# Performance work log

Measured on AMD Instinct MI355X. Metric: run time of the kernel, lower is better.

## Reference

```python
import jax, jax.numpy as jnp
import numpy as np

NUM_BANDS = 8
WINDOW = 2048
OVERLAP = 1024
SR = 16000


def _band_mask(L):
    # Replicates torch: band = searchsorted(band_ranges, |freq|, left) - 1.
    # DC bin gives band=-1 which torch negative-indexes into the LAST band,
    # hence the mod. All bins satisfy band < NUM_BANDS, so all are assigned.
    freqs = np.fft.fftfreq(L, 1.0 / SR)
    ranges = np.linspace(0.0, SR / 2.0, NUM_BANDS + 1)
    idx = np.searchsorted(ranges, np.abs(freqs), side='left') - 1
    idx = idx % NUM_BANDS
    mask = (idx[None, :] == np.arange(NUM_BANDS)[:, None]).astype(np.float32)
    return jnp.asarray(mask)  # [bands, L]


def _band_signals(x):
    # mag*exp(i*phase) of masked bins == masked complex bins; ifft().real per band
    L = x.shape[-1]
    X = jnp.fft.fft(x)                         # [B, L] complex
    mask = _band_mask(L)                       # [bands, L]
    Xb = X[:, None, :] * mask[None, :, :]      # [B, bands, L]
    return jnp.fft.ifft(Xb).real               # [B, bands, L]


def _chunks(sig):
    L = sig.shape[-1]
    hop = WINDOW - OVERLAP
    n = (L - OVERLAP) // hop                   # num_chunks (static)
    idx = (jnp.arange(n) * hop)[:, None] + jnp.arange(WINDOW)[None, :]  # [n, W]
    return sig[:, :, idx]                       # [B, bands, n, W]


def _loudness(x):
    # BS.1770-style energy loudness (vectorized stand-in for the repo's
    # undefined `loudness` helper): -0.691 + 10*log10(mean square)
    ms = jnp.mean(x * x, axis=-1)
    return -0.691 + 10.0 * jnp.log10(ms + 1e-12)


def reference(watermarked_signals, original_signals):
    ro = _band_signals(original_signals)
    rw = _band_signals(watermarked_signals)
    lo = _loudness(_chunks(ro))                # [B, bands, n]
    lw = _loudness(_chunks(rw))
    lo = jnp.where(jnp.isnan(lo), 0.0, lo)
    lw = jnp.where(jnp.isnan(lw), 0.0, lw)
    diff = (lw - lo).reshape(-1)               # ordered (i, j, k) like the torch loop
    w = jax.nn.softmax(diff)
    return jnp.sum(w * diff)


def setup_inputs() -> dict:
    key = jax.random.key(0)
    k1, k2 = jax.random.split(key)
    B, L = 8, 160000
    return {
        'watermarked_signals': jax.random.normal(k1, (B, L), dtype=jnp.float32),
        'original_signals': jax.random.normal(k2, (B, L), dtype=jnp.float32),
    }
```

## Files before the change

### kernel.cpp

```cpp
#include <hip/hip_runtime.h>
#include <hip/hip_fp16.h>
#include <math.h>

constexpr int L      = 160000;
constexpr int BATCH  = 8;
constexpr int NB     = 8;
constexpr int NHOPS  = 156;
constexpr int NCHUNK = 155;
constexpr int RS     = 289;
constexpr float TWO_PI = 6.28318530717958647692f;
constexpr float INVL = 1.0f / (float)L;

__device__ __forceinline__ float2 cmulf(float2 a, float2 b) {
  return make_float2(a.x * b.x - a.y * b.y, a.x * b.y + a.y * b.x);
}

__device__ __forceinline__ float2 cisf(float a) {
  float s, c;
  __sincosf(a, &s, &c);
  return make_float2(c, s);
}

__device__ __forceinline__ float2 conjf(float2 a) { return make_float2(a.x, -a.y); }

__device__ __forceinline__ int pad8(int i) { return i + (i >> 3); }

template <int SIGN>
__device__ __forceinline__ void bf4s(float2* v) {
  float2 t0 = make_float2(v[0].x + v[2].x, v[0].y + v[2].y);
  float2 t1 = make_float2(v[0].x - v[2].x, v[0].y - v[2].y);
  float2 t2 = make_float2(v[1].x + v[3].x, v[1].y + v[3].y);
  float2 t3 = make_float2(v[1].x - v[3].x, v[1].y - v[3].y);
  v[0] = make_float2(t0.x + t2.x, t0.y + t2.y);
  v[2] = make_float2(t0.x - t2.x, t0.y - t2.y);
  if constexpr (SIGN < 0) {
    v[1] = make_float2(t1.x + t3.y, t1.y - t3.x);
    v[3] = make_float2(t1.x - t3.y, t1.y + t3.x);
  } else {
    v[1] = make_float2(t1.x - t3.y, t1.y + t3.x);
    v[3] = make_float2(t1.x + t3.y, t1.y - t3.x);
  }
}

template <int SIGN>
__device__ __forceinline__ void bf5s(float2* v) {
  const float c1 = 0.30901699437494745f, s1 = 0.9510565162951535f;
  const float c2 = -0.8090169943749475f, s2 = 0.5877852522924731f;
  float2 t1 = make_float2(v[1].x + v[4].x, v[1].y + v[4].y);
  float2 t3 = make_float2(v[1].x - v[4].x, v[1].y - v[4].y);
  float2 t2 = make_float2(v[2].x + v[3].x, v[2].y + v[3].y);
  float2 t4 = make_float2(v[2].x - v[3].x, v[2].y - v[3].y);
  float2 a = make_float2(v[0].x + c1 * t1.x + c2 * t2.x, v[0].y + c1 * t1.y + c2 * t2.y);
  float2 b = make_float2(s1 * t3.x + s2 * t4.x, s1 * t3.y + s2 * t4.y);
  float2 c = make_float2(v[0].x + c2 * t1.x + c1 * t2.x, v[0].y + c2 * t1.y + c1 * t2.y);
  float2 d = make_float2(s2 * t3.x - s1 * t4.x, s2 * t3.y - s1 * t4.y);
  v[0] = make_float2(v[0].x + t1.x + t2.x, v[0].y + t1.y + t2.y);
  if constexpr (SIGN < 0) {
    v[1] = make_float2(a.x + b.y, a.y - b.x);
    v[4] = make_float2(a.x - b.y, a.y + b.x);
    v[2] = make_float2(c.x + d.y, c.y - d.x);
    v[3] = make_float2(c.x - d.y, c.y + d.x);
  } else {
    v[1] = make_float2(a.x - b.y, a.y + b.x);
    v[4] = make_float2(a.x + b.y, a.y - b.x);
    v[2] = make_float2(c.x - d.y, c.y + d.x);
    v[3] = make_float2(c.x + d.y, c.y - d.x);
  }
}

template <int R>
__device__ __forceinline__ void twchain(float2* v, float2 t1) {
  float2 t = t1;
  v[1] = cmulf(v[1], t);
#pragma unroll
  for (int r = 2; r < R; ++r) { t = cmulf(t, t1); v[r] = cmulf(v[r], t); }
}

__device__ __forceinline__ int rev3_5(int q) {
  int q5 = q / 5, q25 = q / 25;
  int d0 = q - 5 * q5, d1 = q5 - 5 * q25;
  return 25 * d0 + 5 * d1 + q25;
}

__device__ __forceinline__ int rev3_4(int q) {
  return ((q & 3) << 4) | (q & 12) | (q >> 4);
}

template <int SUB, int SIGN>
__device__ __forceinline__ void dif5_ip_stage_c(float2* a, int ln) {
  int i1 = ln, i2 = ln + 64;
  bool g2 = (i2 < 125);
  int j1 = i1 % SUB, j2 = i2 % SUB;
  int b1 = (i1 / SUB) * (5 * SUB) + j1;
  int b2 = (i2 / SUB) * (5 * SUB) + j2;
  float2 u[5], v[5];
#pragma unroll
  for (int r = 0; r < 5; ++r) u[r] = a[b1 + SUB * r];
  if (g2) {
#pragma unroll
    for (int r = 0; r < 5; ++r) v[r] = a[b2 + SUB * r];
  }
  bf5s<SIGN>(u);
  twchain<5>(u, cisf((float)SIGN * (TWO_PI / (float)(5 * SUB)) * (float)j1));
  if (g2) {
    bf5s<SIGN>(v);
    twchain<5>(v, cisf((float)SIGN * (TWO_PI / (float)(5 * SUB)) * (float)j2));
  }
#pragma unroll
  for (int r = 0; r < 5; ++r) a[b1 + SUB * r] = u[r];
  if (g2) {
#pragma unroll
    for (int r = 0; r < 5; ++r) a[b2 + SUB * r] = v[r];
  }
}

template <int SUB>
__device__ __forceinline__ void dif5_ip_stage_t(float2* a, int ln, float2 t1a, float2 t1b) {
  int i1 = ln, i2 = ln + 64;
  bool g2 = (i2 < 125);
  int j1 = i1 % SUB, j2 = i2 % SUB;
  int b1 = (i1 / SUB) * (5 * SUB) + j1;
  int b2 = (i2 / SUB) * (5 * SUB) + j2;
  float2 u[5], v[5];
#pragma unroll
  for (int r = 0; r < 5; ++r) u[r] = a[b1 + SUB * r];
  if (g2) {
#pragma unroll
    for (int r = 0; r < 5; ++r) v[r] = a[b2 + SUB * r];
  }
  bf5s<1>(u);
  twchain<5>(u, t1a);
  if (g2) {
    bf5s<1>(v);
    twchain<5>(v, t1b);
  }
#pragma unroll
  for (int r = 0; r < 5; ++r) a[b1 + SUB * r] = u[r];
  if (g2) {
#pragma unroll
    for (int r = 0; r < 5; ++r) a[b2 + SUB * r] = v[r];
  }
}

template <int SIGN>
__device__ __forceinline__ void dif625_ip(float2* a, int ln) {
  dif5_ip_stage_c<125, SIGN>(a, ln);
  dif5_ip_stage_c<25, SIGN>(a, ln);
  dif5_ip_stage_c<5, SIGN>(a, ln);
  int q1 = ln, q2 = ln + 64;
  bool g2 = (q2 < 125);
  float2 u[5], v[5];
#pragma unroll
  for (int r = 0; r < 5; ++r) u[r] = a[5 * q1 + r];
  if (g2) {
#pragma unroll
    for (int r = 0; r < 5; ++r) v[r] = a[5 * q2 + r];
  }
  bf5s<SIGN>(u);
  if (g2) bf5s<SIGN>(v);
  int rv1 = rev3_5(q1), rv2 = rev3_5(q2);
#pragma unroll
  for (int r = 0; r < 5; ++r) a[125 * r + rv1] = u[r];
  if (g2) {
#pragma unroll
    for (int r = 0; r < 5; ++r) a[125 * r + rv2] = v[r];
  }
}

template <int SIGN>
__device__ __forceinline__ void dif256sw_tw(float2* a, int ln,
                                            float2 tw1, float2 tw2, float2 tw3) {
  {
    int b = pad8(ln);
    float2 u[4];
#pragma unroll
    for (int r = 0; r < 4; ++r) u[r] = a[b + 72 * r];
    bf4s<SIGN>(u);
    twchain<4>(u, tw1);
#pragma unroll
    for (int r = 0; r < 4; ++r) a[b + 72 * r] = u[r];
  }
  {
    int j = ln & 15, b = pad8(64 * (ln >> 4) + j);
    float2 u[4];
#pragma unroll
    for (int r = 0; r < 4; ++r) u[r] = a[b + 18 * r];
    bf4s<SIGN>(u);
    twchain<4>(u, tw2);
#pragma unroll
    for (int r = 0; r < 4; ++r) a[b + 18 * r] = u[r];
  }
  {
    int j = ln & 3, jb = 16 * (ln >> 2) + j;
    float2 u[4];
#pragma unroll
    for (int r = 0; r < 4; ++r) u[r] = a[pad8(jb + 4 * r)];
    bf4s<SIGN>(u);
    twchain<4>(u, tw3);
#pragma unroll
    for (int r = 0; r < 4; ++r) a[pad8(jb + 4 * r)] = u[r];
  }
  {
    float2 u[4];
#pragma unroll
    for (int r = 0; r < 4; ++r) u[r] = a[pad8(4 * ln + r)];
    bf4s<SIGN>(u);
    int rv = rev3_4(ln);
#pragma unroll
    for (int r = 0; r < 4; ++r) a[pad8(64 * r + rv)] = u[r];
  }
}

__global__ __launch_bounds__(256) void f1_kernel(const float* __restrict__ win,
                                                 const float* __restrict__ oin,
                                                 float2* __restrict__ G,
                                                 float* __restrict__ E) {
  __shared__ float2 A[4 * 625];
  int blk = blockIdx.x;
  int gid = blk * 256 + threadIdx.x;
  if (gid < 2 * BATCH * NB * NHOPS) E[gid] = 0.0f;
  int sig = blk >> 6, g = blk & 63;
  int n1base = g * 4;
  int tid = threadIdx.x;
  const float4* wp4 = (const float4*)(win + (size_t)sig * L);
  const float4* op4 = (const float4*)(oin + (size_t)sig * L);
  for (int r = tid; r < 625; r += 256) {
    float4 wv = wp4[r * 64 + g];
    float4 ov = op4[r * 64 + g];
    A[0 * 625 + r] = make_float2(wv.x, ov.x);
    A[1 * 625 + r] = make_float2(wv.y, ov.y);
    A[2 * 625 + r] = make_float2(wv.z, ov.z);
    A[3 * 625 + r] = make_float2(wv.w, ov.w);
  }
  __syncthreads();
  int wv_ = tid >> 6, ln = tid & 63;
  dif625_ip<-1>(A + wv_ * 625, ln);
  __syncthreads();
  int cc = tid & 3, k20 = tid >> 2;
  int n1 = n1base + cc;
  float w = -(TWO_PI / (float)L) * (float)n1;
  float2 t = cisf(w * (float)k20);
  float2 stp = cisf(w * 64.0f);
  for (int k2 = k20; k2 < 625; k2 += 64) {
    G[(size_t)sig * L + k2 * 256 + n1] = cmulf(A[cc * 625 + k2], t);
    t = cmulf(t, stp);
  }
}

__global__ __launch_bounds__(1024) void fi_kernel(const float2* __restrict__ G,
                                                  __half2* __restrict__ H) {
  __shared__ float2 Xb[16 * RS];
  __shared__ float2 Wb[16 * RS];
  int blk = blockIdx.x;
  int bg  = blk / (BATCH * 40);
  int rem = blk - bg * (BATCH * 40);
  int sig = rem / 40, gr = rem % 40;
  int k2base = gr * 16;
  int tid = threadIdx.x;
  int wv = tid >> 6, ln = tid & 63;
  int k2 = k2base + wv;
  bool act = (k2 < 625);
  float2* xr = Xb + wv * RS;
  float2* wr = Wb + wv * RS;

  float2 tw1 = cisf((TWO_PI / 256.0f) * (float)ln);
  float2 tw2 = cisf((TWO_PI / 64.0f) * (float)(ln & 15));
  float2 tw3 = cisf((TWO_PI / 16.0f) * (float)(ln & 3));

  if (act) {
#pragma unroll
    for (int r = 0; r < 4; ++r)
      xr[pad8(ln + 64 * r)] = G[(size_t)sig * L + k2 * 256 + ln + 64 * r];
    dif256sw_tw<-1>(xr, ln, conjf(tw1), conjf(tw2), conjf(tw3));
  }

  int b1 = pad8(ln);
  int b2 = pad8(64 * (ln >> 4) + (ln & 15));
  int jb3 = 16 * (ln >> 2) + (ln & 3);
  int kb = 625 * ln + k2;

  int cc = tid & 15, q = tid >> 4;
  int rq = rev3_4(q);
  int k2e = k2base + cc;
  bool eact = (k2e < 625);
  float a0 = (TWO_PI / (float)L) * (float)k2e;
  float2 t0q = cisf(a0 * (float)rq);
  float2 stp = cisf(a0 * 64.0f);
  int b4 = cc * RS + pad8(4 * q);

#pragma unroll
  for (int bi = 0; bi < 2; ++bi) {
    int band = bg * 2 + bi;
    unsigned lo1, d1, lo2, d2;
    if (band < 7) {
      lo1 = 10000u * band + 1u;              d1 = 9999u;
      lo2 = (unsigned)L - 10000u * (band + 1); d2 = 9999u;
    } else {
      lo1 = 70001u; d1 = 19998u;
      lo2 = 0u;     d2 = 0u;
    }
    if (act) {
      float2 u[4];
#pragma unroll
      for (int r = 0; r < 4; ++r) {
        float2 x = xr[b1 + 72 * r];
        unsigned k = (unsigned)(kb + 40000 * r);
        bool in = ((k - lo1) <= d1) || ((k - lo2) <= d2);
        u[r] = in ? x : make_float2(0.0f, 0.0f);
      }
      bf4s<1>(u);
      twchain<4>(u, tw1);
#pragma unroll
      for (int r = 0; r < 4; ++r) wr[b1 + 72 * r] = u[r];
#pragma unroll
      for (int r = 0; r < 4; ++r) u[r] = wr[b2 + 18 * r];
      bf4s<1>(u);
      twchain<4>(u, tw2);
#pragma unroll
      for (int r = 0; r < 4; ++r) wr[b2 + 18 * r] = u[r];
#pragma unroll
      for (int r = 0; r < 4; ++r) u[r] = wr[pad8(jb3 + 4 * r)];
      bf4s<1>(u);
      twchain<4>(u, tw3);
#pragma unroll
      for (int r = 0; r < 4; ++r) wr[pad8(jb3 + 4 * r)] = u[r];
    }
    __syncthreads();
    if (eact) {
      size_t obase = (size_t)(sig * NB + band) * L;
      float2 v[4];
#pragma unroll
      for (int r = 0; r < 4; ++r) v[r] = Wb[b4 + r];
      bf4s<1>(v);
      float2 t = t0q;
#pragma unroll
      for (int r = 0; r < 4; ++r) {
        int n1 = 64 * r + rq;
        float2 val = cmulf(v[r], t);
        H[obase + (size_t)n1 * 625 + k2e] = __floats2half2_rn(val.x * INVL, val.y * INVL);
        t = cmulf(t, stp);
      }
    }
    __syncthreads();
  }
}

__global__ __launch_bounds__(256) void i2_kernel(const __half2* __restrict__ H,
                                                 float* __restrict__ E) {
  __shared__ float2 A[4 * 625];
  __shared__ float P[4 * 2 * NHOPS];
  int blk = blockIdx.x;
  int g = blk & 31, sb = blk >> 5;
  int band = sb & 7, sig = sb >> 3;
  int tid = threadIdx.x;
  int wv = tid >> 6, ln = tid & 63;
  size_t base = (size_t)(sig * NB + band) * L;
  int n1A = 8 * g + wv, n1B = 8 * g + 4 + wv;
  const __half2* HA = H + base + (size_t)n1A * 625;
  const __half2* HB = H + base + (size_t)n1B * 625;
  int j1 = ln, j2 = ln + 64;
  bool g2 = (j2 < 125);
  __half2 hA1[5], hA2[5], hB1[5], hB2[5];
#pragma unroll
  for (int r = 0; r < 5; ++r) hA1[r] = HA[j1 + 125 * r];
  if (g2) {
#pragma unroll
    for (int r = 0; r < 5; ++r) hA2[r] = HA[j2 + 125 * r];
  }
#pragma unroll
  for (int r = 0; r < 5; ++r) hB1[r] = HB[j1 + 125 * r];
  if (g2) {
#pragma unroll
    for (int r = 0; r < 5; ++r) hB2[r] = HB[j2 + 125 * r];
  }
  float2 tS1a = cisf((TWO_PI / 625.0f) * (float)j1);
  float2 tS1b = cisf((TWO_PI / 625.0f) * (float)j2);
  float2 tS2a = cisf((TWO_PI / 125.0f) * (float)(j1 % 25));
  float2 tS2b = cisf((TWO_PI / 125.0f) * (float)(j2 % 25));
  float2 tS3a = cisf((TWO_PI / 25.0f) * (float)(j1 % 5));
  float2 tS3b = cisf((TWO_PI / 25.0f) * (float)(j2 % 5));
  float2* a = A + wv * 625;
  float* Pw = P + wv * (2 * NHOPS);

  {
    float2 u[5];
#pragma unroll
    for (int r = 0; r < 5; ++r) u[r] = __half22float2(hA1[r]);
    bf5s<1>(u);
    twchain<5>(u, tS1a);
#pragma unroll
    for (int r = 0; r < 5; ++r) a[j1 + 125 * r] = u[r];
    if (g2) {
      float2 v[5];
#pragma unroll
      for (int r = 0; r < 5; ++r) v[r] = __half22float2(hA2[r]);
      bf5s<1>(v);
      twchain<5>(v, tS1b);
#pragma unroll
      for (int r = 0; r < 5; ++r) a[j2 + 125 * r] = v[r];
    }
  }
  dif5_ip_stage_t<25>(a, ln, tS2a, tS2b);
  dif5_ip_stage_t<5>(a, ln, tS3a, tS3b);
  {
    float2 u[5], v[5];
#pragma unroll
    for (int r = 0; r < 5; ++r) u[r] = a[5 * j1 + r];
    if (g2) {
#pragma unroll
      for (int r = 0; r < 5; ++r) v[r] = a[5 * j2 + r];
    }
    bf5s<1>(u);
    if (g2) bf5s<1>(v);
    int rv1 = rev3_5(j1), rv2 = rev3_5(j2);
#pragma unroll
    for (int r = 0; r < 5; ++r) a[125 * r + rv1] = u[r];
    if (g2) {
#pragma unroll
      for (int r = 0; r < 5; ++r) a[125 * r + rv2] = v[r];
    }
  }
  for (int h = ln; h < NHOPS; h += 64) {
    float ex = 0.0f, ey = 0.0f;
#pragma unroll
    for (int d = 0; d < 4; ++d) {
      float2 z = a[4 * h + d];
      ex += z.x * z.x;
      ey += z.y * z.y;
    }
    Pw[h] = ex;
    Pw[NHOPS + h] = ey;
  }

  {
    float2 u[5];
#pragma unroll
    for (int r = 0; r < 5; ++r) u[r] = __half22float2(hB1[r]);
    bf5s<1>(u);
    twchain<5>(u, tS1a);
#pragma unroll
    for (int r = 0; r < 5; ++r) a[j1 + 125 * r] = u[r];
    if (g2) {
      float2 v[5];
#pragma unroll
      for (int r = 0; r < 5; ++r) v[r] = __half22float2(hB2[r]);
      bf5s<1>(v);
      twchain<5>(v, tS1b);
#pragma unroll
      for (int r = 0; r < 5; ++r) a[j2 + 125 * r] = v[r];
    }
  }
  dif5_ip_stage_t<25>(a, ln, tS2a, tS2b);
  dif5_ip_stage_t<5>(a, ln, tS3a, tS3b);
  {
    float2 u[5], v[5];
#pragma unroll
    for (int r = 0; r < 5; ++r) u[r] = a[5 * j1 + r];
    if (g2) {
#pragma unroll
      for (int r = 0; r < 5; ++r) v[r] = a[5 * j2 + r];
    }
    bf5s<1>(u);
    if (g2) bf5s<1>(v);
    int rv1 = rev3_5(j1), rv2 = rev3_5(j2);
#pragma unroll
    for (int r = 0; r < 5; ++r) a[125 * r + rv1] = u[r];
    if (g2) {
#pragma unroll
      for (int r = 0; r < 5; ++r) a[125 * r + rv2] = v[r];
    }
  }
  for (int h = ln; h < NHOPS; h += 64) {
    float ex = 0.0f, ey = 0.0f;
#pragma unroll
    for (int d = 0; d < 4; ++d) {
      float2 z = a[4 * h + d];
      ex += z.x * z.x;
      ey += z.y * z.y;
    }
    Pw[h] += ex;
    Pw[NHOPS + h] += ey;
  }
  __syncthreads();
  int eb = (sig * NB + band) * NHOPS;
  for (int idx = tid; idx < 2 * NHOPS; idx += 256) {
    float v = P[idx] + P[2 * NHOPS + idx] + P[4 * NHOPS + idx] + P[6 * NHOPS + idx];
    int comp = idx / NHOPS, h = idx - comp * NHOPS;
    atomicAdd(&E[comp * (BATCH * NB * NHOPS) + eb + h], v);
  }
}

__global__ __launch_bounds__(1024) void finalize_kernel(const float* __restrict__ E,
                                                        float* __restrict__ out) {
  constexpr int ND = BATCH * NB * NCHUNK;
  constexpr float SC = 1.0f / 2048.0f;
  __shared__ float diffs[ND];
  __shared__ float sred[1024];
  int tid = threadIdx.x;
  for (int idx = tid; idx < ND; idx += 1024) {
    int sb = idx / NCHUNK;
    int k = idx - sb * NCHUNK;
    float msw = (E[sb * NHOPS + k] + E[sb * NHOPS + k + 1]) * SC;
    float mso = (E[64 * NHOPS + sb * NHOPS + k] + E[64 * NHOPS + sb * NHOPS + k + 1]) * SC;
    float lw = -0.691f + 10.0f * log10f(msw + 1e-12f);
    float lo = -0.691f + 10.0f * log10f(mso + 1e-12f);
    diffs[idx] = lw - lo;
  }
  __syncthreads();
  float mx = -3.4e38f;
  for (int idx = tid; idx < ND; idx += 1024) mx = fmaxf(mx, diffs[idx]);
  sred[tid] = mx;
  __syncthreads();
  for (int s = 512; s > 0; s >>= 1) {
    if (tid < s) sred[tid] = fmaxf(sred[tid], sred[tid + s]);
    __syncthreads();
  }
  float gmax = sred[0];
  __syncthreads();
  float se = 0.0f, swd = 0.0f;
  for (int idx = tid; idx < ND; idx += 1024) {
    float d = diffs[idx];
    float e = expf(d - gmax);
    se += e;
    swd += d * e;
  }
  sred[tid] = se; __syncthreads();
  for (int s = 512; s > 0; s >>= 1) { if (tid < s) sred[tid] += sred[tid + s]; __syncthreads(); }
  float tot = sred[0];
  __syncthreads();
  sred[tid] = swd; __syncthreads();
  for (int s = 512; s > 0; s >>= 1) { if (tid < s) sred[tid] += sred[tid + s]; __syncthreads(); }
  if (tid == 0) out[0] = sred[0] / tot;
}

extern "C" void kernel_launch(void* const* d_in, const int* in_sizes, int n_in,
                              void* d_out, int out_size, void* d_ws, size_t ws_size,
                              hipStream_t stream) {
  (void)in_sizes; (void)n_in; (void)out_size; (void)ws_size;
  char* ws = (char*)d_ws;
  float2*  G = (float2*)ws;
  __half2* H = (__half2*)(ws + 10240000);
  float*   E = (float*)(ws + 51200000);
  const float* w = (const float*)d_in[0];
  const float* o = (const float*)d_in[1];

  f1_kernel<<<dim3(BATCH * 64), dim3(256), 0, stream>>>(w, o, G, E);
  fi_kernel<<<dim3(4 * BATCH * 40), dim3(1024), 0, stream>>>(G, H);
  i2_kernel<<<dim3(BATCH * NB * 32), dim3(256), 0, stream>>>(H, E);
  finalize_kernel<<<dim3(1), dim3(1024), 0, stream>>>(E, (float*)d_out);
}
```

Baseline: 144.1 us.

## Use one butterfly per thread in f1 and interleave two FFTs in i2

Measured after the change: 144.1 us. Within noise of the previous version (-0.0%).

```diff
diff --git a/kernel.cpp b/kernel.cpp
--- a/kernel.cpp
+++ b/kernel.cpp
@@ -87,31 +87,16 @@
 }
 
 template <int SUB, int SIGN>
-__device__ __forceinline__ void dif5_ip_stage_c(float2* a, int ln) {
-  int i1 = ln, i2 = ln + 64;
-  bool g2 = (i2 < 125);
-  int j1 = i1 % SUB, j2 = i2 % SUB;
-  int b1 = (i1 / SUB) * (5 * SUB) + j1;
-  int b2 = (i2 / SUB) * (5 * SUB) + j2;
-  float2 u[5], v[5];
-#pragma unroll
-  for (int r = 0; r < 5; ++r) u[r] = a[b1 + SUB * r];
-  if (g2) {
-#pragma unroll
-    for (int r = 0; r < 5; ++r) v[r] = a[b2 + SUB * r];
-  }
+__device__ __forceinline__ void dif5_stage_1b(float2* a, int idx) {
+  int j = idx % SUB;
+  int b = (idx / SUB) * (5 * SUB) + j;
+  float2 u[5];
+#pragma unroll
+  for (int r = 0; r < 5; ++r) u[r] = a[b + SUB * r];
   bf5s<SIGN>(u);
-  twchain<5>(u, cisf((float)SIGN * (TWO_PI / (float)(5 * SUB)) * (float)j1));
-  if (g2) {
-    bf5s<SIGN>(v);
-    twchain<5>(v, cisf((float)SIGN * (TWO_PI / (float)(5 * SUB)) * (float)j2));
-  }
-#pragma unroll
-  for (int r = 0; r < 5; ++r) a[b1 + SUB * r] = u[r];
-  if (g2) {
-#pragma unroll
-    for (int r = 0; r < 5; ++r) a[b2 + SUB * r] = v[r];
-  }
+  twchain<5>(u, cisf((float)SIGN * (TWO_PI / (float)(5 * SUB)) * (float)j));
+#pragma unroll
+  for (int r = 0; r < 5; ++r) a[b + SUB * r] = u[r];
 }
 
 template <int SUB>
@@ -143,31 +128,6 @@
 }
 
 template <int SIGN>
-__device__ __forceinline__ void dif625_ip(float2* a, int ln) {
-  dif5_ip_stage_c<125, SIGN>(a, ln);
-  dif5_ip_stage_c<25, SIGN>(a, ln);
-  dif5_ip_stage_c<5, SIGN>(a, ln);
-  int q1 = ln, q2 = ln + 64;
-  bool g2 = (q2 < 125);
-  float2 u[5], v[5];
-#pragma unroll
-  for (int r = 0; r < 5; ++r) u[r] = a[5 * q1 + r];
-  if (g2) {
-#pragma unroll
-    for (int r = 0; r < 5; ++r) v[r] = a[5 * q2 + r];
-  }
-  bf5s<SIGN>(u);
-  if (g2) bf5s<SIGN>(v);
-  int rv1 = rev3_5(q1), rv2 = rev3_5(q2);
-#pragma unroll
-  for (int r = 0; r < 5; ++r) a[125 * r + rv1] = u[r];
-  if (g2) {
-#pragma unroll
-    for (int r = 0; r < 5; ++r) a[125 * r + rv2] = v[r];
-  }
-}
-
-template <int SIGN>
 __device__ __forceinline__ void dif256sw_tw(float2* a, int ln,
                                             float2 tw1, float2 tw2, float2 tw3) {
   {
@@ -211,20 +171,20 @@
   }
 }
 
-__global__ __launch_bounds__(256) void f1_kernel(const float* __restrict__ win,
+__global__ __launch_bounds__(512) void f1_kernel(const float* __restrict__ win,
                                                  const float* __restrict__ oin,
                                                  float2* __restrict__ G,
                                                  float* __restrict__ E) {
   __shared__ float2 A[4 * 625];
   int blk = blockIdx.x;
-  int gid = blk * 256 + threadIdx.x;
+  int tid = threadIdx.x;
+  int gid = blk * 512 + tid;
   if (gid < 2 * BATCH * NB * NHOPS) E[gid] = 0.0f;
   int sig = blk >> 6, g = blk & 63;
   int n1base = g * 4;
-  int tid = threadIdx.x;
   const float4* wp4 = (const float4*)(win + (size_t)sig * L);
   const float4* op4 = (const float4*)(oin + (size_t)sig * L);
-  for (int r = tid; r < 625; r += 256) {
+  for (int r = tid; r < 625; r += 512) {
     float4 wv = wp4[r * 64 + g];
     float4 ov = op4[r * 64 + g];
     A[0 * 625 + r] = make_float2(wv.x, ov.x);
@@ -233,15 +193,31 @@
     A[3 * 625 + r] = make_float2(wv.w, ov.w);
   }
   __syncthreads();
-  int wv_ = tid >> 6, ln = tid & 63;
-  dif625_ip<-1>(A + wv_ * 625, ln);
+  int col = tid >> 7, idx = tid & 127;
+  float2* a = A + col * 625;
+  bool act = (idx < 125);
+  if (act) dif5_stage_1b<125, -1>(a, idx);
+  __syncthreads();
+  if (act) dif5_stage_1b<25, -1>(a, idx);
+  __syncthreads();
+  if (act) dif5_stage_1b<5, -1>(a, idx);
+  __syncthreads();
+  if (act) {
+    float2 u[5];
+#pragma unroll
+    for (int r = 0; r < 5; ++r) u[r] = a[5 * idx + r];
+    bf5s<-1>(u);
+    int rv = rev3_5(idx);
+#pragma unroll
+    for (int r = 0; r < 5; ++r) a[125 * r + rv] = u[r];
+  }
   __syncthreads();
   int cc = tid & 3, k20 = tid >> 2;
   int n1 = n1base + cc;
   float w = -(TWO_PI / (float)L) * (float)n1;
   float2 t = cisf(w * (float)k20);
-  float2 stp = cisf(w * 64.0f);
-  for (int k2 = k20; k2 < 625; k2 += 64) {
+  float2 stp = cisf(w * 128.0f);
+  for (int k2 = k20; k2 < 625; k2 += 128) {
     G[(size_t)sig * L + k2 * 256 + n1] = cmulf(A[cc * 625 + k2], t);
     t = cmulf(t, stp);
   }
@@ -286,7 +262,6 @@
   float a0 = (TWO_PI / (float)L) * (float)k2e;
   float2 t0q = cisf(a0 * (float)rq);
   float2 stp = cisf(a0 * 64.0f);
-  int b4 = cc * RS + pad8(4 * q);
 
 #pragma unroll
   for (int bi = 0; bi < 2; ++bi) {
@@ -328,6 +303,7 @@
     __syncthreads();
     if (eact) {
       size_t obase = (size_t)(sig * NB + band) * L;
+      int b4 = cc * RS + pad8(4 * q);
       float2 v[4];
 #pragma unroll
       for (int r = 0; r < 4; ++r) v[r] = Wb[b4 + r];
@@ -347,7 +323,8 @@
 
 __global__ __launch_bounds__(256) void i2_kernel(const __half2* __restrict__ H,
                                                  float* __restrict__ E) {
-  __shared__ float2 A[4 * 625];
+  __shared__ float2 AA[4 * 625];
+  __shared__ float2 AB[4 * 625];
   __shared__ float P[4 * 2 * NHOPS];
   int blk = blockIdx.x;
   int g = blk & 31, sb = blk >> 5;
@@ -379,7 +356,8 @@
   float2 tS2b = cisf((TWO_PI / 125.0f) * (float)(j2 % 25));
   float2 tS3a = cisf((TWO_PI / 25.0f) * (float)(j1 % 5));
   float2 tS3b = cisf((TWO_PI / 25.0f) * (float)(j2 % 5));
-  float2* a = A + wv * 625;
+  float2* aA = AA + wv * 625;
+  float2* aB = AB + wv * 625;
   float* Pw = P + wv * (2 * NHOPS);
 
   {
@@ -389,7 +367,7 @@
     bf5s<1>(u);
     twchain<5>(u, tS1a);
 #pragma unroll
-    for (int r = 0; r < 5; ++r) a[j1 + 125 * r] = u[r];
+    for (int r = 0; r < 5; ++r) aA[j1 + 125 * r] = u[r];
     if (g2) {
       float2 v[5];
 #pragma unroll
@@ -397,89 +375,78 @@
       bf5s<1>(v);
       twchain<5>(v, tS1b);
 #pragma unroll
-      for (int r = 0; r < 5; ++r) a[j2 + 125 * r] = v[r];
-    }
-  }
-  dif5_ip_stage_t<25>(a, ln, tS2a, tS2b);
-  dif5_ip_stage_t<5>(a, ln, tS3a, tS3b);
+      for (int r = 0; r < 5; ++r) aA[j2 + 125 * r] = v[r];
+    }
+  }
+  {
+    float2 u[5];
+#pragma unroll
+    for (int r = 0; r < 5; ++r) u[r] = __half22float2(hB1[r]);
+    bf5s<1>(u);
+    twchain<5>(u, tS1a);
+#pragma unroll
+    for (int r = 0; r < 5; ++r) aB[j1 + 125 * r] = u[r];
+    if (g2) {
+      float2 v[5];
+#pragma unroll
+      for (int r = 0; r < 5; ++r) v[r] = __half22float2(hB2[r]);
+      bf5s<1>(v);
+      twchain<5>(v, tS1b);
+#pragma unroll
+      for (int r = 0; r < 5; ++r) aB[j2 + 125 * r] = v[r];
+    }
+  }
+  dif5_ip_stage_t<25>(aA, ln, tS2a, tS2b);
+  dif5_ip_stage_t<25>(aB, ln, tS2a, tS2b);
+  dif5_ip_stage_t<5>(aA, ln, tS3a, tS3b);
+  dif5_ip_stage_t<5>(aB, ln, tS3a, tS3b);
   {
     float2 u[5], v[5];
 #pragma unroll
-    for (int r = 0; r < 5; ++r) u[r] = a[5 * j1 + r];
+    for (int r = 0; r < 5; ++r) u[r] = aA[5 * j1 + r];
     if (g2) {
 #pragma unroll
-      for (int r = 0; r < 5; ++r) v[r] = a[5 * j2 + r];
+      for (int r = 0; r < 5; ++r) v[r] = aA[5 * j2 + r];
     }
     bf5s<1>(u);
     if (g2) bf5s<1>(v);
     int rv1 = rev3_5(j1), rv2 = rev3_5(j2);
 #pragma unroll
-    for (int r = 0; r < 5; ++r) a[125 * r + rv1] = u[r];
+    for (int r = 0; r < 5; ++r) aA[125 * r + rv1] = u[r];
     if (g2) {
 #pragma unroll
-      for (int r = 0; r < 5; ++r) a[125 * r + rv2] = v[r];
-    }
-  }
-  for (int h = ln; h < NHOPS; h += 64) {
-    float ex = 0.0f, ey = 0.0f;
-#pragma unroll
-    for (int d = 0; d < 4; ++d) {
-      float2 z = a[4 * h + d];
-      ex += z.x * z.x;
-      ey += z.y * z.y;
-    }
-    Pw[h] = ex;
-    Pw[NHOPS + h] = ey;
-  }
-
-  {
-    float2 u[5];
-#pragma unroll
-    for (int r = 0; r < 5; ++r) u[r] = __half22float2(hB1[r]);
-    bf5s<1>(u);
-    twchain<5>(u, tS1a);
-#pragma unroll
-    for (int r = 0; r < 5; ++r) a[j1 + 125 * r] = u[r];
+      for (int r = 0; r < 5; ++r) aA[125 * r + rv2] = v[r];
+    }
+  }
+  {
+    float2 u[5], v[5];
+#pragma unroll
+    for (int r = 0; r < 5; ++r) u[r] = aB[5 * j1 + r];
     if (g2) {
-      float2 v[5];
-#pragma unroll
-      for (int r = 0; r < 5; ++r) v[r] = __half22float2(hB2[r]);
-      bf5s<1>(v);
-      twchain<5>(v, tS1b);
-#pragma unroll
-      for (int r = 0; r < 5; ++r) a[j2 + 125 * r] = v[r];
-    }
-  }
-  dif5_ip_stage_t<25>(a, ln, tS2a, tS2b);
-  dif5_ip_stage_t<5>(a, ln, tS3a, tS3b);
-  {
-    float2 u[5], v[5];
-#pragma unroll
-    for (int r = 0; r < 5; ++r) u[r] = a[5 * j1 + r];
-    if (g2) {
-#pragma unroll
-      for (int r = 0; r < 5; ++r) v[r] = a[5 * j2 + r];
+#pragma unroll
+      for (int r = 0; r < 5; ++r) v[r] = aB[5 * j2 + r];
     }
     bf5s<1>(u);
     if (g2) bf5s<1>(v);
     int rv1 = rev3_5(j1), rv2 = rev3_5(j2);
 #pragma unroll
-    for (int r = 0; r < 5; ++r) a[125 * r + rv1] = u[r];
+    for (int r = 0; r < 5; ++r) aB[125 * r + rv1] = u[r];
     if (g2) {
 #pragma unroll
-      for (int r = 0; r < 5; ++r) a[125 * r + rv2] = v[r];
+      for (int r = 0; r < 5; ++r) aB[125 * r + rv2] = v[r];
     }
   }
   for (int h = ln; h < NHOPS; h += 64) {
     float ex = 0.0f, ey = 0.0f;
 #pragma unroll
     for (int d = 0; d < 4; ++d) {
-      float2 z = a[4 * h + d];
-      ex += z.x * z.x;
-      ey += z.y * z.y;
-    }
-    Pw[h] += ex;
-    Pw[NHOPS + h] += ey;
+      float2 zA = aA[4 * h + d];
+      float2 zB = aB[4 * h + d];
+      ex += zA.x * zA.x + zB.x * zB.x;
+      ey += zA.y * zA.y + zB.y * zB.y;
+    }
+    Pw[h] = ex;
+    Pw[NHOPS + h] = ey;
   }
   __syncthreads();
   int eb = (sig * NB + band) * NHOPS;
@@ -544,7 +511,7 @@
   const float* w = (const float*)d_in[0];
   const float* o = (const float*)d_in[1];
 
-  f1_kernel<<<dim3(BATCH * 64), dim3(256), 0, stream>>>(w, o, G, E);
+  f1_kernel<<<dim3(BATCH * 64), dim3(512), 0, stream>>>(w, o, G, E);
   fi_kernel<<<dim3(4 * BATCH * 40), dim3(1024), 0, stream>>>(G, H);
   i2_kernel<<<dim3(BATCH * NB * 32), dim3(256), 0, stream>>>(H, E);
   finalize_kernel<<<dim3(1), dim3(1024), 0, stream>>>(E, (float*)d_out);
```
